# Kernel optimization log

Hardware: AMD Instinct MI355X
Metric: run time of the kernel (lower is better)

## Reference

```python
import jax, jax.numpy as jnp
import numpy as np

DIM = 1024
HEADS = 16
HEAD_DIM = DIM // HEADS
N_CLUSTERS = 8
B, N = 4, 1024


def setup_inputs() -> dict:
    key = jax.random.key(0)
    ks = jax.random.split(key, 10)
    s = 0.02
    return {
        "x": jax.random.normal(ks[0], (B, N, DIM), dtype=jnp.float32),
        "Wqkv": jax.random.normal(ks[1], (DIM, 3 * DIM), dtype=jnp.float32) * s,
        "Wproj": jax.random.normal(ks[2], (DIM, DIM), dtype=jnp.float32) * s,
        "bproj": jnp.zeros((DIM,), dtype=jnp.float32),
        "Wgroup": jax.random.normal(ks[3], (HEAD_DIM, N_CLUSTERS), dtype=jnp.float32) * s,
        "bgroup": jnp.zeros((N_CLUSTERS,), dtype=jnp.float32),
        "Wtheta": jax.random.normal(ks[4], (HEAD_DIM, 1), dtype=jnp.float32) * s,
        "btheta": jnp.zeros((1,), dtype=jnp.float32),
        "affinity_B": jax.random.normal(ks[5], (HEADS, N_CLUSTERS, N_CLUSTERS), dtype=jnp.float32),
        "cp_bias_scale": jnp.asarray(1.0, dtype=jnp.float32),
        "flag": 1,
        "injection": 0,
        "cp_dcmm": 1,
    }


def reference(x, Wqkv, Wproj, bproj, Wgroup, bgroup, Wtheta, btheta,
              affinity_B, cp_bias_scale, flag, injection, cp_dcmm):
    b, n, c = x.shape
    h = affinity_B.shape[0]
    hd = c // h
    scale = hd ** -0.5
    # qkv: [b,n,3c] -> [3,b,h,n,hd]
    qkv = (x @ Wqkv).reshape(b, n, 3, h, hd).transpose(2, 0, 3, 1, 4)
    q, k, v = qkv[0], qkv[1], qkv[2]
    attn = jnp.einsum('bhnd,bhmd->bhnm', q, k) * scale
    z_constraint = jnp.asarray(0.0, dtype=x.dtype)
    if cp_dcmm and flag:
        # cluster assignments per query token
        z = jax.nn.softmax(q @ Wgroup + bgroup, axis=-1)          # [b,h,n,K]
        B_aff = jax.nn.sigmoid(affinity_B)                         # [h,K,K]
        zB = jnp.einsum('bhik,hkl->bhil', z, B_aff)
        cp_bias_ori = jnp.tanh(jnp.einsum('bhil,bhjl->bhij', zB, z))  # [b,h,n,n]
        theta = jax.nn.relu(jnp.squeeze(q @ Wtheta + btheta, -1))  # [b,h,n]
        degree_term = theta[..., :, None] * theta[..., None, :]
        cp_bias = cp_bias_scale * degree_term * cp_bias_ori
        attn = attn + cp_bias
        z_constraint = -(z * jnp.log(z + 1e-8)).sum(axis=-1).mean()
    else:
        cp_bias = jnp.zeros_like(attn)
    attn = jax.nn.softmax(attn, axis=-1)
    out = jnp.einsum('bhnm,bhmd->bhnd', attn, v).transpose(0, 2, 1, 3).reshape(b, n, c)
    out = out @ Wproj + bproj
    zero = jnp.asarray(0.0, dtype=x.dtype)
    return (out, z_constraint, zero, zero, cp_bias)
```

## Files before the change

### kernel.cpp

```cpp
#include <hip/hip_runtime.h>
#include <stdint.h>

#define DIM 1024
#define HEADS 16
#define HD 64
#define NC 8
#define BB 4
#define NN 1024
#define ROWS (BB*NN)
#define TOK (BB*HEADS*NN)
#define OUT_OFF_Z (ROWS*DIM)
#define CP_OFF    (ROWS*DIM+3)

typedef __bf16 bf16_t;
typedef __attribute__((ext_vector_type(8))) __bf16 bf16x8;
typedef __attribute__((ext_vector_type(4))) __bf16 bf16x4;
typedef __attribute__((ext_vector_type(4))) float f32x4;

__device__ __forceinline__ void gload16(const void* g, void* l){
#if __has_builtin(__builtin_amdgcn_global_load_lds)
  __builtin_amdgcn_global_load_lds(
      (__attribute__((address_space(1))) void*)(g),
      (__attribute__((address_space(3))) void*)(l), 16, 0, 0);
#else
  *(uint4*)l = *(const uint4*)g;
#endif
}

__device__ __forceinline__ float tanh_poly(float d){
  float t2 = d*d;
  float p = -0.33333333f + t2*(0.13333333f + t2*(-0.05396825f));
  return d*(1.f + t2*p);
}

__global__ __launch_bounds__(256) void prep_kernel(
    const float* __restrict__ x, const float* __restrict__ Wqkv,
    const float* __restrict__ Wproj, const float* __restrict__ affB,
    bf16_t* __restrict__ xb, bf16_t* __restrict__ WqkvT, bf16_t* __restrict__ WprojT,
    float* __restrict__ sigB, float* __restrict__ out_scalars){
  const int bid = blockIdx.x, tid = threadIdx.x;
  if(bid < 4096){
    int i = (bid*256 + tid)*4;
    float4 v = *(const float4*)&x[i];
    bf16x4 o = {(bf16_t)v.x, (bf16_t)v.y, (bf16_t)v.z, (bf16_t)v.w};
    *(bf16x4*)&xb[i] = o;
    return;
  }
  if(bid < 8192){
    __shared__ float tile[32][33];
    const float* in; bf16_t* out; int K, N, bx, by;
    if(bid < 7168){ int t = bid-4096; in = Wqkv;  out = WqkvT;  K = 1024; N = 3072; bx = t%96; by = t/96; }
    else          { int t = bid-7168; in = Wproj; out = WprojT; K = 1024; N = 1024; bx = t%32; by = t/32; }
    int k0 = by*32, n0 = bx*32;
    int tx = tid & 31, ty = tid >> 5;
    #pragma unroll
    for(int r=ty; r<32; r+=8) tile[r][tx] = in[(size_t)(k0+r)*N + n0+tx];
    __syncthreads();
    #pragma unroll
    for(int r=ty; r<32; r+=8) out[(size_t)(n0+r)*K + k0+tx] = (bf16_t)tile[tx][r];
    return;
  }
  #pragma unroll
  for(int r=0;r<4;r++){
    int i = r*256 + tid;
    sigB[i] = 1.f/(1.f + __expf(-affB[i]));
  }
  if(tid < 3) out_scalars[tid] = 0.f;
}

__global__ __launch_bounds__(256) void gemm_qkvt(const bf16_t* __restrict__ xb,
                                                 const bf16_t* __restrict__ WT,
                                                 bf16_t* __restrict__ Qb,
                                                 bf16_t* __restrict__ Kb,
                                                 bf16_t* __restrict__ Vt){
  const int K = DIM;
  __shared__ __align__(16) bf16_t As[128*32];
  __shared__ __align__(16) bf16_t Bs[128*32];
  const int bid = blockIdx.x, tid = threadIdx.x;
  const bool qkmode = bid < 512;
  int m0, n0;
  const bf16_t *Ap, *Bp;
  if(qkmode){ m0 = (bid>>4)*128;            n0 = (bid&15)*128;
              Ap = xb + (size_t)m0*K;       Bp = WT + (size_t)n0*K; }
  else      { int t = bid-512; m0 = (t>>5)*128; n0 = (t&31)*128;
              Ap = WT + (size_t)(2048+m0)*K; Bp = xb + (size_t)n0*K; }
  const int wave = tid>>6, lane = tid&63, l15 = lane&15, quad = lane>>4;
  const int wm = (wave>>1)*64, wn = (wave&1)*64;

  f32x4 acc[4][4];
  #pragma unroll
  for(int i=0;i<4;i++)
    #pragma unroll
    for(int j=0;j<4;j++) acc[i][j] = (f32x4){0.f,0.f,0.f,0.f};

  for(int k0=0; k0<K; k0+=32){
    #pragma unroll
    for(int p=0;p<2;p++){
      int c = tid + p*256;
      int r = c>>2, s = c&3, xs = s ^ ((r>>1)&3);
      gload16(Ap + (size_t)r*K + k0 + xs*8, &As[c*8]);
      gload16(Bp + (size_t)r*K + k0 + xs*8, &Bs[c*8]);
    }
    __syncthreads();

    bf16x8 a[4], b[4];
    #pragma unroll
    for(int i=0;i<4;i++){
      int R = wm + i*16 + l15;
      a[i] = *(const bf16x8*)&As[R*32 + ((quad ^ ((R>>1)&3)))*8];
    }
    #pragma unroll
    for(int j=0;j<4;j++){
      int R = wn + j*16 + l15;
      b[j] = *(const bf16x8*)&Bs[R*32 + ((quad ^ ((R>>1)&3)))*8];
    }
    #pragma unroll
    for(int i=0;i<4;i++)
      #pragma unroll
      for(int j=0;j<4;j++)
        acc[i][j] = __builtin_amdgcn_mfma_f32_16x16x32_bf16(a[i], b[j], acc[i][j], 0,0,0);
    __syncthreads();
  }

  if(qkmode){
    #pragma unroll
    for(int j=0;j<4;j++){
      int col = n0 + wn + j*16 + l15;
      int which = col>>10, hc = col&1023, h = hc>>6, d = hc&63;
      bf16_t* dst = which ? Kb : Qb;
      #pragma unroll
      for(int i=0;i<4;i++){
        int m = m0 + wm + i*16 + quad*4;
        #pragma unroll
        for(int r=0;r<4;r++){
          int row = m + r;
          int bh = (row>>10)*HEADS + h, n = row&1023;
          dst[((size_t)bh*NN + n)*HD + d] = (bf16_t)acc[i][j][r];
        }
      }
    }
  } else {
    const int b = n0 >> 10;
    #pragma unroll
    for(int i=0;i<4;i++)
      #pragma unroll
      for(int j=0;j<4;j++){
        int vcol = m0 + wm + i*16 + quad*4;
        int ncol = (n0 & 1023) + wn + j*16 + l15;
        #pragma unroll
        for(int r=0;r<4;r++)
          Vt[((size_t)(b*1024 + vcol + r))*NN + ncol] = (bf16_t)acc[i][j][r];
      }
  }
}

__global__ __launch_bounds__(256) void token_kernel(
    const bf16_t* __restrict__ Qb, const float* __restrict__ Wgroup,
    const float* __restrict__ bgroup, const float* __restrict__ Wtheta,
    const float* __restrict__ btheta, const float* __restrict__ sigB,
    bf16_t* __restrict__ zb16, bf16_t* __restrict__ zBb16,
    float* __restrict__ thetaAll, float* __restrict__ entPart){
  const int bid = blockIdx.x, tid = threadIdx.x;
  const int t = bid*256 + tid;
  const int h = (t>>10)&15;
  __shared__ float Wg[64][NC];
  __shared__ float Wt[64];
  __shared__ float sB[64];
  __shared__ float bg[NC];
  if(tid < 64){
    #pragma unroll
    for(int c=0;c<NC;c++) Wg[tid][c] = Wgroup[tid*NC + c];
    Wt[tid] = Wtheta[tid];
    sB[tid] = sigB[h*64 + tid];
  }
  if(tid < NC) bg[tid] = bgroup[tid];
  __syncthreads();

  float zl[8] = {0,0,0,0,0,0,0,0};
  float th = 0.f;
  const bf16_t* qrow = Qb + (size_t)t*HD;
  #pragma unroll
  for(int v=0; v<8; v++){
    bf16x8 qv = *(const bf16x8*)&qrow[v*8];
    #pragma unroll
    for(int e=0;e<8;e++){
      float qd = (float)qv[e];
      int d = v*8+e;
      #pragma unroll
      for(int c=0;c<8;c++) zl[c] += qd * Wg[d][c];
      th += qd * Wt[d];
    }
  }
  th = fmaxf(th + btheta[0], 0.f);
  #pragma unroll
  for(int c=0;c<8;c++) zl[c] += bg[c];

  float mx = zl[0];
  #pragma unroll
  for(int c=1;c<8;c++) mx = fmaxf(mx, zl[c]);
  float ssum = 0.f;
  #pragma unroll
  for(int c=0;c<8;c++){ zl[c] = __expf(zl[c]-mx); ssum += zl[c]; }
  float inv = 1.f/ssum;
  float ent = 0.f;
  #pragma unroll
  for(int c=0;c<8;c++){ float z = zl[c]*inv; zl[c] = z; ent -= z*__logf(z + 1e-8f); }

  float zb[8];
  #pragma unroll
  for(int l=0;l<8;l++){
    float a = 0.f;
    #pragma unroll
    for(int k2=0;k2<8;k2++) a += zl[k2]*sB[k2*8 + l];
    zb[l] = a;
  }
  bf16x8 zv, zbv;
  #pragma unroll
  for(int c=0;c<8;c++){ zv[c] = (bf16_t)zl[c]; zbv[c] = (bf16_t)zb[c]; }
  *(bf16x8*)&zb16[(size_t)t*8]  = zv;
  *(bf16x8*)&zBb16[(size_t)t*8] = zbv;
  thetaAll[t] = th;

  ent += __shfl_xor(ent,1);  ent += __shfl_xor(ent,2);  ent += __shfl_xor(ent,4);
  ent += __shfl_xor(ent,8);  ent += __shfl_xor(ent,16); ent += __shfl_xor(ent,32);
  __shared__ float es[4];
  if((tid&63)==0) es[tid>>6] = ent;
  __syncthreads();
  if(tid==0) entPart[bid] = es[0]+es[1]+es[2]+es[3];
}

__global__ __launch_bounds__(256) void attn_kernel(
    const bf16_t* __restrict__ Qb, const bf16_t* __restrict__ Kb,
    const bf16_t* __restrict__ Vt, const bf16_t* __restrict__ zb16,
    const bf16_t* __restrict__ zBb16, const float* __restrict__ thetaAll,
    const float* __restrict__ cps_p, float* __restrict__ cp_out,
    bf16_t* __restrict__ attnO){
  const int bid = blockIdx.x;
  const int tid = threadIdx.x;
  const int wave = tid>>6, lane = tid&63, l15 = lane&15, quad = lane>>4;
  const float cps = cps_p[0];

  __shared__ __align__(16) bf16_t Qs[128*64];
  __shared__ __align__(16) bf16_t Ks[64*64];
  __shared__ __align__(16) bf16_t Vs[64*64];
  __shared__ __align__(16) bf16_t Ps[4][16*72];
  __shared__ float thAll[NN];

  if(bid >= 512){
    const int b2 = bid - 512;
    const int bh = b2 & 63, qt = b2 >> 6;
    { float4 tv = *(const float4*)&thetaAll[(size_t)bh*NN + tid*4];
      *(float4*)&thAll[tid*4] = tv; }
    bf16x8 aZ = (bf16x8)(bf16_t)0.f;
    if(quad==0)
      aZ = *(const bf16x8*)&zBb16[((size_t)bh*NN + qt*64 + wave*16 + l15)*8];
    __syncthreads();
    float th_i[4];
    #pragma unroll
    for(int r=0;r<4;r++) th_i[r] = thAll[qt*64 + wave*16 + quad*4 + r];

    for(int kt=0; kt<16; ++kt){
      #pragma unroll
      for(int f=0;f<4;f++){
        bf16x8 bz = (bf16x8)(bf16_t)0.f;
        if(quad==0)
          bz = *(const bf16x8*)&zb16[((size_t)bh*NN + kt*64 + f*16 + l15)*8];
        f32x4 D = __builtin_amdgcn_mfma_f32_16x16x32_bf16(aZ, bz,
                    (f32x4){0.f,0.f,0.f,0.f}, 0,0,0);
        float thj = thAll[kt*64 + f*16 + l15];
        #pragma unroll
        for(int r=0;r<4;r++){
          float bv = cps * th_i[r] * thj * tanh_poly(D[r]);
          int irow = qt*64 + wave*16 + quad*4 + r;
          cp_out[((size_t)bh*NN + irow)*NN + (size_t)kt*64 + f*16 + l15] = bv;
        }
      }
    }
    return;
  }

  const int bh = bid & 63, qt = bid >> 6;
  const int b = bh >> 4, h = bh & 15;

  {
    const bf16_t* Qg = Qb + ((size_t)bh*NN + (size_t)qt*128)*HD;
    #pragma unroll
    for(int p=0;p<4;p++){
      int c = tid + p*256;
      int r = c>>3, xs = (c&7) ^ (r&7);
      gload16(Qg + r*64 + xs*8, &Qs[c*8]);
    }
    float4 tv = *(const float4*)&thetaAll[(size_t)bh*NN + tid*4];
    *(float4*)&thAll[tid*4] = tv;
  }
  bf16x8 aZ[2];
  #pragma unroll
  for(int qf=0;qf<2;qf++){
    aZ[qf] = (bf16x8)(bf16_t)0.f;
    if(quad==0)
      aZ[qf] = *(const bf16x8*)&zBb16[((size_t)bh*NN + qt*128 + wave*32 + qf*16 + l15)*8];
  }
  __syncthreads();

  float th_i[2][4];
  bf16x8 aq[2][2];
  #pragma unroll
  for(int qf=0;qf<2;qf++){
    int row = wave*32 + qf*16 + l15;
    aq[qf][0] = *(const bf16x8*)&Qs[row*64 + ((quad  ) ^ (row&7))*8];
    aq[qf][1] = *(const bf16x8*)&Qs[row*64 + ((quad+4) ^ (row&7))*8];
    #pragma unroll
    for(int r=0;r<4;r++)
      th_i[qf][r] = thAll[qt*128 + wave*32 + qf*16 + quad*4 + r];
  }

  float l_r[2][4] = {{0.f,0.f,0.f,0.f},{0.f,0.f,0.f,0.f}};
  f32x4 o[2][4];
  #pragma unroll
  for(int qf=0;qf<2;qf++)
    #pragma unroll
    for(int dn=0;dn<4;dn++) o[qf][dn] = (f32x4){0.f,0.f,0.f,0.f};

  for(int kt=0; kt<16; ++kt){
    const bf16_t* Kg = Kb + ((size_t)bh*NN + (size_t)kt*64)*HD;
    #pragma unroll
    for(int p=0;p<2;p++){
      int c = tid + p*256;
      int r = c>>3, xs = (c&7) ^ (r&7);
      gload16(Kg + r*64 + xs*8, &Ks[c*8]);
    }
    #pragma unroll
    for(int p=0;p<2;p++){
      int c = tid + p*256;
      int r = c>>3, xs = (c&7) ^ (r&7);
      gload16(Vt + (size_t)(bh*HD + r)*NN + kt*64 + xs*8, &Vs[c*8]);
    }

    float biasv[2][4][4];
    #pragma unroll
    for(int f=0;f<4;f++){
      bf16x8 bz = (bf16x8)(bf16_t)0.f;
      if(quad==0)
        bz = *(const bf16x8*)&zb16[((size_t)bh*NN + kt*64 + f*16 + l15)*8];
      float thj = thAll[kt*64 + f*16 + l15];
      #pragma unroll
      for(int qf=0;qf<2;qf++){
        f32x4 D = __builtin_amdgcn_mfma_f32_16x16x32_bf16(aZ[qf], bz,
                    (f32x4){0.f,0.f,0.f,0.f}, 0,0,0);
        #pragma unroll
        for(int r=0;r<4;r++)
          biasv[qf][f][r] = cps * th_i[qf][r] * thj * tanh_poly(D[r]);
      }
    }
    __syncthreads();

    #pragma unroll
    for(int qf=0;qf<2;qf++){
      f32x4 s[4];
      float rs[4] = {0.f,0.f,0.f,0.f};
      #pragma unroll
      for(int f=0;f<4;f++){
        int row = f*16 + l15;
        f32x4 z4 = (f32x4){0.f,0.f,0.f,0.f};
        bf16x8 b0 = *(const bf16x8*)&Ks[row*64 + ((quad  ) ^ (row&7))*8];
        bf16x8 b1 = *(const bf16x8*)&Ks[row*64 + ((quad+4) ^ (row&7))*8];
        z4 = __builtin_amdgcn_mfma_f32_16x16x32_bf16(aq[qf][0], b0, z4, 0,0,0);
        z4 = __builtin_amdgcn_mfma_f32_16x16x32_bf16(aq[qf][1], b1, z4, 0,0,0);
        #pragma unroll
        for(int r=0;r<4;r++){
          float p = __expf(z4[r]*0.125f + biasv[qf][f][r]);
          z4[r] = p;
          rs[r] += p;
        }
        s[f] = z4;
      }
      #pragma unroll
      for(int r=0;r<4;r++){
        float v = rs[r];
        v += __shfl_xor(v,1); v += __shfl_xor(v,2);
        v += __shfl_xor(v,4); v += __shfl_xor(v,8);
        l_r[qf][r] += v;
      }

      #pragma unroll
      for(int f=0;f<4;f++)
        #pragma unroll
        for(int r=0;r<4;r++)
          Ps[wave][(quad*4+r)*72 + f*16 + l15] = (bf16_t)s[f][r];

      bf16x8 pa0 = *(const bf16x8*)&Ps[wave][l15*72 + quad*8];
      bf16x8 pa1 = *(const bf16x8*)&Ps[wave][l15*72 + 32 + quad*8];
      #pragma unroll
      for(int dn=0;dn<4;dn++){
        int row = dn*16 + l15;
        bf16x8 b0 = *(const bf16x8*)&Vs[row*64 + ((quad  ) ^ (row&7))*8];
        bf16x8 b1 = *(const bf16x8*)&Vs[row*64 + ((quad+4) ^ (row&7))*8];
        o[qf][dn] = __builtin_amdgcn_mfma_f32_16x16x32_bf16(pa0, b0, o[qf][dn], 0,0,0);
        o[qf][dn] = __builtin_amdgcn_mfma_f32_16x16x32_bf16(pa1, b1, o[qf][dn], 0,0,0);
      }
    }
    __syncthreads();
  }

  #pragma unroll
  for(int qf=0;qf<2;qf++)
    #pragma unroll
    for(int r=0;r<4;r++){
      float inv = 1.f / l_r[qf][r];
      int grow = qt*128 + wave*32 + qf*16 + quad*4 + r;
      #pragma unroll
      for(int dn=0;dn<4;dn++)
        attnO[((size_t)(b*NN + grow))*DIM + h*HD + dn*16 + l15] = (bf16_t)(o[qf][dn][r]*inv);
    }
}

__global__ __launch_bounds__(256) void gemm_proj_ent(const bf16_t* __restrict__ A,
                                                     const bf16_t* __restrict__ Bt,
                                                     float* __restrict__ C,
                                                     const float* __restrict__ bias,
                                                     const float* __restrict__ entPart,
                                                     float* __restrict__ outz){
  const int bid = blockIdx.x, tid = threadIdx.x;
  if(bid == 512){
    float s = (tid < 256) ? entPart[tid] : 0.f;
    s += __shfl_xor(s,1); s += __shfl_xor(s,2); s += __shfl_xor(s,4);
    s += __shfl_xor(s,8); s += __shfl_xor(s,16); s += __shfl_xor(s,32);
    __shared__ float ls[4];
    if((tid&63)==0) ls[tid>>6] = s;
    __syncthreads();
    if(tid==0) outz[0] = (ls[0]+ls[1]+ls[2]+ls[3]) * (1.0f/(float)TOK);
    return;
  }
  const int K = DIM, N = DIM;
  __shared__ __align__(16) bf16_t As[128*32];
  __shared__ __align__(16) bf16_t Bs[64*32];
  const int m0 = (bid>>4)*128, n0 = (bid&15)*64;
  const int wave = tid>>6, lane = tid&63, l15 = lane&15, quad = lane>>4;
  const int wm = (wave>>1)*64, wn = (wave&1)*32;

  f32x4 acc[4][2];
  #pragma unroll
  for(int i=0;i<4;i++)
    #pragma unroll
    for(int j=0;j<2;j++) acc[i][j] = (f32x4){0.f,0.f,0.f,0.f};

  for(int k0=0; k0<K; k0+=32){
    {
      int c = tid;
      int r = c>>2, s = c&3, xs = s ^ ((r>>1)&3);
      gload16(A  + (size_t)(m0 + r)*K + k0 + xs*8, &As[c*8]);
      gload16(Bt + (size_t)(n0 + r)*K + k0 + xs*8, &Bs[c*8]);
      c = tid + 256;
      r = c>>2; s = c&3; xs = s ^ ((r>>1)&3);
      gload16(A  + (size_t)(m0 + r)*K + k0 + xs*8, &As[c*8]);
    }
    __syncthreads();

    bf16x8 a[4], b[2];
    #pragma unroll
    for(int i=0;i<4;i++){
      int R = wm + i*16 + l15;
      a[i] = *(const bf16x8*)&As[R*32 + ((quad ^ ((R>>1)&3)))*8];
    }
    #pragma unroll
    for(int j=0;j<2;j++){
      int R = wn + j*16 + l15;
      b[j] = *(const bf16x8*)&Bs[R*32 + ((quad ^ ((R>>1)&3)))*8];
    }
    #pragma unroll
    for(int i=0;i<4;i++)
      #pragma unroll
      for(int j=0;j<2;j++)
        acc[i][j] = __builtin_amdgcn_mfma_f32_16x16x32_bf16(a[i], b[j], acc[i][j], 0,0,0);
    __syncthreads();
  }

  #pragma unroll
  for(int i=0;i<4;i++)
    #pragma unroll
    for(int j=0;j<2;j++){
      int row = m0 + wm + i*16 + quad*4;
      int col = n0 + wn + j*16 + l15;
      float bv = bias[col];
      #pragma unroll
      for(int r=0;r<4;r++)
        C[(size_t)(row+r)*N + col] = acc[i][j][r] + bv;
    }
}

extern "C" void kernel_launch(void* const* d_in, const int* in_sizes, int n_in,
                              void* d_out, int out_size, void* d_ws, size_t ws_size,
                              hipStream_t stream){
  const float* x      = (const float*)d_in[0];
  const float* Wqkv   = (const float*)d_in[1];
  const float* Wproj  = (const float*)d_in[2];
  const float* bproj  = (const float*)d_in[3];
  const float* Wgroup = (const float*)d_in[4];
  const float* bgroup = (const float*)d_in[5];
  const float* Wtheta = (const float*)d_in[6];
  const float* btheta = (const float*)d_in[7];
  const float* affB   = (const float*)d_in[8];
  const float* cps    = (const float*)d_in[9];
  float* out = (float*)d_out;
  char* ws = (char*)d_ws;

  bf16_t* xb       = (bf16_t*)(ws);
  bf16_t* WqkvT    = (bf16_t*)(ws + (size_t)8*1048576);
  bf16_t* WprojT   = (bf16_t*)(ws + (size_t)14*1048576);
  bf16_t* Qb       = (bf16_t*)(ws + (size_t)16*1048576);
  bf16_t* Kb       = (bf16_t*)(ws + (size_t)24*1048576);
  bf16_t* Vt       = (bf16_t*)(ws + (size_t)32*1048576);
  bf16_t* zb16     = (bf16_t*)(ws + (size_t)40*1048576);
  bf16_t* zBb16    = (bf16_t*)(ws + (size_t)41*1048576);
  float*  thetaAll = (float*) (ws + (size_t)42*1048576);
  float*  entPart  = (float*) (ws + (size_t)43*1048576);
  bf16_t* attnO    = (bf16_t*)(ws + (size_t)44*1048576);
  float*  sigB     = (float*) (ws + (size_t)52*1048576);

  prep_kernel<<<8193, 256, 0, stream>>>(x, Wqkv, Wproj, affB, xb, WqkvT, WprojT,
                                        sigB, out + OUT_OFF_Z);
  gemm_qkvt<<<768, 256, 0, stream>>>(xb, WqkvT, Qb, Kb, Vt);
  token_kernel<<<256, 256, 0, stream>>>(Qb, Wgroup, bgroup, Wtheta, btheta, sigB,
                                        zb16, zBb16, thetaAll, entPart);
  attn_kernel<<<1536, 256, 0, stream>>>(Qb, Kb, Vt, zb16, zBb16, thetaAll,
                                        cps, out + CP_OFF, attnO);
  gemm_proj_ent<<<513, 256, 0, stream>>>(attnO, WprojT, out, bproj,
                                         entPart, out + OUT_OFF_Z);
}
```

Measured before the change: 478.5 us.

## Double-buffer K/V tiles in attention and widen QKV GEMM k-tile

```diff
diff --git a/kernel.cpp b/kernel.cpp
--- a/kernel.cpp
+++ b/kernel.cpp
@@ -74,8 +74,8 @@
                                                  bf16_t* __restrict__ Kb,
                                                  bf16_t* __restrict__ Vt){
   const int K = DIM;
-  __shared__ __align__(16) bf16_t As[128*32];
-  __shared__ __align__(16) bf16_t Bs[128*32];
+  __shared__ __align__(16) bf16_t As[128*64];
+  __shared__ __align__(16) bf16_t Bs[128*64];
   const int bid = blockIdx.x, tid = threadIdx.x;
   const bool qkmode = bid < 512;
   int m0, n0;
@@ -93,32 +93,35 @@
     #pragma unroll
     for(int j=0;j<4;j++) acc[i][j] = (f32x4){0.f,0.f,0.f,0.f};
 
-  for(int k0=0; k0<K; k0+=32){
-    #pragma unroll
-    for(int p=0;p<2;p++){
+  for(int k0=0; k0<K; k0+=64){
+    #pragma unroll
+    for(int p=0;p<4;p++){
       int c = tid + p*256;
-      int r = c>>2, s = c&3, xs = s ^ ((r>>1)&3);
+      int r = c>>3, s = c&7, xs = s ^ (r&7);
       gload16(Ap + (size_t)r*K + k0 + xs*8, &As[c*8]);
       gload16(Bp + (size_t)r*K + k0 + xs*8, &Bs[c*8]);
     }
     __syncthreads();
 
-    bf16x8 a[4], b[4];
-    #pragma unroll
-    for(int i=0;i<4;i++){
-      int R = wm + i*16 + l15;
-      a[i] = *(const bf16x8*)&As[R*32 + ((quad ^ ((R>>1)&3)))*8];
-    }
-    #pragma unroll
-    for(int j=0;j<4;j++){
-      int R = wn + j*16 + l15;
-      b[j] = *(const bf16x8*)&Bs[R*32 + ((quad ^ ((R>>1)&3)))*8];
-    }
-    #pragma unroll
-    for(int i=0;i<4;i++)
-      #pragma unroll
-      for(int j=0;j<4;j++)
-        acc[i][j] = __builtin_amdgcn_mfma_f32_16x16x32_bf16(a[i], b[j], acc[i][j], 0,0,0);
+    #pragma unroll
+    for(int kc=0;kc<2;kc++){
+      bf16x8 a[4], b[4];
+      #pragma unroll
+      for(int i=0;i<4;i++){
+        int R = wm + i*16 + l15;
+        a[i] = *(const bf16x8*)&As[R*64 + ((kc*4+quad) ^ (R&7))*8];
+      }
+      #pragma unroll
+      for(int j=0;j<4;j++){
+        int R = wn + j*16 + l15;
+        b[j] = *(const bf16x8*)&Bs[R*64 + ((kc*4+quad) ^ (R&7))*8];
+      }
+      #pragma unroll
+      for(int i=0;i<4;i++)
+        #pragma unroll
+        for(int j=0;j<4;j++)
+          acc[i][j] = __builtin_amdgcn_mfma_f32_16x16x32_bf16(a[i], b[j], acc[i][j], 0,0,0);
+    }
     __syncthreads();
   }
 
@@ -240,10 +243,8 @@
   const int wave = tid>>6, lane = tid&63, l15 = lane&15, quad = lane>>4;
   const float cps = cps_p[0];
 
-  __shared__ __align__(16) bf16_t Qs[128*64];
-  __shared__ __align__(16) bf16_t Ks[64*64];
-  __shared__ __align__(16) bf16_t Vs[64*64];
-  __shared__ __align__(16) bf16_t Ps[4][16*72];
+  __shared__ __align__(16) bf16_t QsPs[128*64];
+  __shared__ __align__(16) bf16_t KV[2][2][64*64];
   __shared__ float thAll[NN];
 
   if(bid >= 512){
@@ -282,17 +283,34 @@
   const int bh = bid & 63, qt = bid >> 6;
   const int b = bh >> 4, h = bh & 15;
 
+  auto stageKV = [&](int buf, int kt){
+    const bf16_t* Kg = Kb + ((size_t)bh*NN + (size_t)kt*64)*HD;
+    #pragma unroll
+    for(int p=0;p<2;p++){
+      int c = tid + p*256;
+      int r = c>>3, xs = (c&7) ^ (r&7);
+      gload16(Kg + r*64 + xs*8, &KV[buf][0][c*8]);
+    }
+    #pragma unroll
+    for(int p=0;p<2;p++){
+      int c = tid + p*256;
+      int r = c>>3, xs = (c&7) ^ (r&7);
+      gload16(Vt + (size_t)(bh*HD + r)*NN + kt*64 + xs*8, &KV[buf][1][c*8]);
+    }
+  };
+
   {
     const bf16_t* Qg = Qb + ((size_t)bh*NN + (size_t)qt*128)*HD;
     #pragma unroll
     for(int p=0;p<4;p++){
       int c = tid + p*256;
       int r = c>>3, xs = (c&7) ^ (r&7);
-      gload16(Qg + r*64 + xs*8, &Qs[c*8]);
+      gload16(Qg + r*64 + xs*8, &QsPs[c*8]);
     }
     float4 tv = *(const float4*)&thetaAll[(size_t)bh*NN + tid*4];
     *(float4*)&thAll[tid*4] = tv;
   }
+  stageKV(0, 0);
   bf16x8 aZ[2];
   #pragma unroll
   for(int qf=0;qf<2;qf++){
@@ -307,12 +325,13 @@
   #pragma unroll
   for(int qf=0;qf<2;qf++){
     int row = wave*32 + qf*16 + l15;
-    aq[qf][0] = *(const bf16x8*)&Qs[row*64 + ((quad  ) ^ (row&7))*8];
-    aq[qf][1] = *(const bf16x8*)&Qs[row*64 + ((quad+4) ^ (row&7))*8];
+    aq[qf][0] = *(const bf16x8*)&QsPs[row*64 + ((quad  ) ^ (row&7))*8];
+    aq[qf][1] = *(const bf16x8*)&QsPs[row*64 + ((quad+4) ^ (row&7))*8];
     #pragma unroll
     for(int r=0;r<4;r++)
       th_i[qf][r] = thAll[qt*128 + wave*32 + qf*16 + quad*4 + r];
   }
+  bf16_t* Ps = &QsPs[wave*(16*72)];
 
   float l_r[2][4] = {{0.f,0.f,0.f,0.f},{0.f,0.f,0.f,0.f}};
   f32x4 o[2][4];
@@ -322,19 +341,9 @@
     for(int dn=0;dn<4;dn++) o[qf][dn] = (f32x4){0.f,0.f,0.f,0.f};
 
   for(int kt=0; kt<16; ++kt){
-    const bf16_t* Kg = Kb + ((size_t)bh*NN + (size_t)kt*64)*HD;
-    #pragma unroll
-    for(int p=0;p<2;p++){
-      int c = tid + p*256;
-      int r = c>>3, xs = (c&7) ^ (r&7);
-      gload16(Kg + r*64 + xs*8, &Ks[c*8]);
-    }
-    #pragma unroll
-    for(int p=0;p<2;p++){
-      int c = tid + p*256;
-      int r = c>>3, xs = (c&7) ^ (r&7);
-      gload16(Vt + (size_t)(bh*HD + r)*NN + kt*64 + xs*8, &Vs[c*8]);
-    }
+    const int cur = kt&1;
+    if(kt > 0) __syncthreads();
+    if(kt+1 < 16) stageKV(1-cur, kt+1);
 
     float biasv[2][4][4];
     #pragma unroll
@@ -352,8 +361,9 @@
           biasv[qf][f][r] = cps * th_i[qf][r] * thj * tanh_poly(D[r]);
       }
     }
-    __syncthreads();
-
+
+    const bf16_t* Ksb = KV[cur][0];
+    const bf16_t* Vsb = KV[cur][1];
     #pragma unroll
     for(int qf=0;qf<2;qf++){
       f32x4 s[4];
@@ -362,8 +372,8 @@
       for(int f=0;f<4;f++){
         int row = f*16 + l15;
         f32x4 z4 = (f32x4){0.f,0.f,0.f,0.f};
-        bf16x8 b0 = *(const bf16x8*)&Ks[row*64 + ((quad  ) ^ (row&7))*8];
-        bf16x8 b1 = *(const bf16x8*)&Ks[row*64 + ((quad+4) ^ (row&7))*8];
+        bf16x8 b0 = *(const bf16x8*)&Ksb[row*64 + ((quad  ) ^ (row&7))*8];
+        bf16x8 b1 = *(const bf16x8*)&Ksb[row*64 + ((quad+4) ^ (row&7))*8];
         z4 = __builtin_amdgcn_mfma_f32_16x16x32_bf16(aq[qf][0], b0, z4, 0,0,0);
         z4 = __builtin_amdgcn_mfma_f32_16x16x32_bf16(aq[qf][1], b1, z4, 0,0,0);
         #pragma unroll
@@ -386,20 +396,19 @@
       for(int f=0;f<4;f++)
         #pragma unroll
         for(int r=0;r<4;r++)
-          Ps[wave][(quad*4+r)*72 + f*16 + l15] = (bf16_t)s[f][r];
-
-      bf16x8 pa0 = *(const bf16x8*)&Ps[wave][l15*72 + quad*8];
-      bf16x8 pa1 = *(const bf16x8*)&Ps[wave][l15*72 + 32 + quad*8];
+          Ps[(quad*4+r)*72 + f*16 + l15] = (bf16_t)s[f][r];
+
+      bf16x8 pa0 = *(const bf16x8*)&Ps[l15*72 + quad*8];
+      bf16x8 pa1 = *(const bf16x8*)&Ps[l15*72 + 32 + quad*8];
       #pragma unroll
       for(int dn=0;dn<4;dn++){
         int row = dn*16 + l15;
-        bf16x8 b0 = *(const bf16x8*)&Vs[row*64 + ((quad  ) ^ (row&7))*8];
-        bf16x8 b1 = *(const bf16x8*)&Vs[row*64 + ((quad+4) ^ (row&7))*8];
+        bf16x8 b0 = *(const bf16x8*)&Vsb[row*64 + ((quad  ) ^ (row&7))*8];
+        bf16x8 b1 = *(const bf16x8*)&Vsb[row*64 + ((quad+4) ^ (row&7))*8];
         o[qf][dn] = __builtin_amdgcn_mfma_f32_16x16x32_bf16(pa0, b0, o[qf][dn], 0,0,0);
         o[qf][dn] = __builtin_amdgcn_mfma_f32_16x16x32_bf16(pa1, b1, o[qf][dn], 0,0,0);
       }
     }
-    __syncthreads();
   }
 
   #pragma unroll
```

Measured after the change: 480.7 us. No clear change (+0.5%).
